# Optimization experiments

Hardware: AMD Instinct MI355X
Metric: run time of the kernel (lower is better)

## Reference

```python
import jax, jax.numpy as jnp
import numpy as np

B, T, D, HD = 256, 256, 512, 64  # batch, seq_len(SEQ_LEN), EMBED_DIM, head_dim


def setup_inputs() -> dict:
    key = jax.random.key(0)
    k1, k2, k3, k4 = jax.random.split(key, 4)
    scale = D ** -0.5  # roughly matches nn.Linear init variance
    return {
        "x": jax.random.normal(k1, (B, T, D), dtype=jnp.float32),
        "Wq": jax.random.normal(k2, (HD, D), dtype=jnp.float32) * scale,
        "Wk": jax.random.normal(k3, (HD, D), dtype=jnp.float32) * scale,
        "Wv": jax.random.normal(k4, (HD, D), dtype=jnp.float32) * scale,
    }


def reference(x, Wq, Wk, Wv):
    # q,k,v: [B, T, HD]  (torch Linear: x @ W.T, no bias)
    q = jnp.einsum("btd,hd->bth", x, Wq)
    k = jnp.einsum("btd,hd->bth", x, Wk)
    v = jnp.einsum("btd,hd->bth", x, Wv)
    head_dim = Wq.shape[0]
    # scores: [B, T, T], scaled by head_dim^-0.5
    scores = jnp.einsum("bqh,bkh->bqk", q, k) * (head_dim ** -0.5)
    T_ = x.shape[1]
    causal = jnp.tril(jnp.ones((T_, T_), dtype=bool))  # tril[:T,:T] == 0 -> -inf
    scores = jnp.where(causal, scores, -jnp.inf)
    attn = jax.nn.softmax(scores, axis=-1)
    # dropout is identity in eval mode (reference baseline)
    return jnp.einsum("bqk,bkh->bqh", attn, v)
```

## Files before the change

### kernel.cpp

```cpp
#include <hip/hip_runtime.h>
#include <hip/hip_bf16.h>
#include <stdint.h>

#define NB 256
#define NT 256
#define ND 512
#define NH 64

typedef __bf16 bf16;
typedef __bf16 bf16x4 __attribute__((ext_vector_type(4)));
typedef __bf16 bf16x8 __attribute__((ext_vector_type(8)));
typedef float f32x4 __attribute__((ext_vector_type(4)));

static __device__ __forceinline__ f32x4 mfma16(bf16x8 a, bf16x8 b, f32x4 c) {
    return __builtin_amdgcn_mfma_f32_16x16x32_bf16(a, b, c, 0, 0, 0);
}

static __device__ __forceinline__ bf16x8 cvt8(f32x4 a, f32x4 b) {
    bf16x8 r;
    r[0] = (bf16)a.x; r[1] = (bf16)a.y; r[2] = (bf16)a.z; r[3] = (bf16)a.w;
    r[4] = (bf16)b.x; r[5] = (bf16)b.y; r[6] = (bf16)b.z; r[7] = (bf16)b.w;
    return r;
}

static __device__ __forceinline__ void gload_lds16(const void* g, void* l) {
    __builtin_amdgcn_global_load_lds(
        (const __attribute__((address_space(1))) void*)g,
        (__attribute__((address_space(3))) void*)l, 16, 0, 0);
}

__global__ __launch_bounds__(256) void wconv_kernel(
        const float* __restrict__ Wq, const float* __restrict__ Wk,
        const float* __restrict__ Wv, bf16* __restrict__ wbf) {
    int idx = (blockIdx.x * 256 + threadIdx.x) * 4;
    const float* src;
    if (idx < 64 * ND)       src = Wq + idx;
    else if (idx < 128 * ND) src = Wk + (idx - 64 * ND);
    else                     src = Wv + (idx - 128 * ND);
    f32x4 v = *reinterpret_cast<const f32x4*>(src);
    bf16x4 o;
    o[0] = (bf16)v.x; o[1] = (bf16)v.y; o[2] = (bf16)v.z; o[3] = (bf16)v.w;
    *reinterpret_cast<bf16x4*>(wbf + idx) = o;
}

__global__ __launch_bounds__(256, 4) void qkv_gemm_kernel(
        const float* __restrict__ x, const bf16* __restrict__ wbf,
        bf16* __restrict__ qws, bf16* __restrict__ kws, bf16* __restrict__ vt) {
    __shared__ alignas(16) char lds[32768];
    const int t = threadIdx.x, lane = t & 63, wave = t >> 6;
    const int l15 = lane & 15, g = lane >> 4;
    const long m0 = (long)blockIdx.x * 64;
    const char* xb = (const char*)x;

    f32x4 acc[4][3] = {};

    #pragma unroll
    for (int i = 0; i < 4; ++i) {
        int row = wave * 16 + i * 4 + g;
        const char* src = xb + (m0 + row) * 2048 + ((l15 * 16) ^ ((row & 7) << 4));
        gload_lds16(src, lds + (wave * 4 + i) * 1024);
    }
    asm volatile("s_waitcnt vmcnt(0)");
    __syncthreads();

    #pragma unroll
    for (int s = 0; s < 8; ++s) {
        const int cbuf = (s & 1) * 16384;
        if (s < 7) {
            const int nbuf = ((s + 1) & 1) * 16384;
            #pragma unroll
            for (int i = 0; i < 4; ++i) {
                int row = wave * 16 + i * 4 + g;
                const char* src = xb + (m0 + row) * 2048 + (long)(s + 1) * 256
                                + ((l15 * 16) ^ ((row & 7) << 4));
                gload_lds16(src, lds + nbuf + (wave * 4 + i) * 1024);
            }
        }
        #pragma unroll
        for (int k2 = 0; k2 < 2; ++k2) {
            const int cbyte = (k2 * 32 + g * 8) * 4;
            bf16x8 Af[4];
            #pragma unroll
            for (int ri = 0; ri < 4; ++ri) {
                int row = ri * 16 + l15;
                int sw = (row & 7) << 4;
                f32x4 lo = *reinterpret_cast<const f32x4*>(lds + cbuf + row * 256 + (cbyte ^ sw));
                f32x4 hi = *reinterpret_cast<const f32x4*>(lds + cbuf + row * 256 + ((cbyte + 16) ^ sw));
                Af[ri] = cvt8(lo, hi);
            }
            const int kg = s * 64 + k2 * 32 + g * 8;
            #pragma unroll
            for (int ci = 0; ci < 3; ++ci) {
                int n = wave * 48 + ci * 16 + l15;
                bf16x8 Bf = *reinterpret_cast<const bf16x8*>(wbf + n * ND + kg);
                #pragma unroll
                for (int ri = 0; ri < 4; ++ri)
                    acc[ri][ci] = mfma16(Af[ri], Bf, acc[ri][ci]);
            }
        }
        asm volatile("s_waitcnt vmcnt(0)");
        __syncthreads();
    }

    const int b = blockIdx.x >> 2;
    const int tb = (blockIdx.x & 3) * 64;
    #pragma unroll
    for (int ci = 0; ci < 3; ++ci) {
        int n = wave * 48 + ci * 16 + l15;
        int sel = n >> 6, hd = n & 63;
        #pragma unroll
        for (int ri = 0; ri < 4; ++ri) {
            #pragma unroll
            for (int r = 0; r < 4; ++r) {
                int trow = tb + ri * 16 + g * 4 + r;
                long grow = m0 + ri * 16 + g * 4 + r;
                float val = acc[ri][ci][r];
                if (sel == 0)      qws[grow * NH + hd] = (bf16)(val * 0.125f);
                else if (sel == 1) kws[grow * NH + hd] = (bf16)val;
                else               vt[((long)b * NH + hd) * NT + trow] = (bf16)val;
            }
        }
    }
}

__global__ __launch_bounds__(256) void attn_kernel(
        const bf16* __restrict__ qws, const bf16* __restrict__ kws,
        const bf16* __restrict__ vt, float* __restrict__ out) {
    __shared__ alignas(16) char lds[65536];
    const int t = threadIdx.x, lane = t & 63, wave = t >> 6;
    const int l15 = lane & 15, g = lane >> 4;
    const int b = blockIdx.x;
    const long bbase = (long)b * NT;

    {
        const bf16* src = kws + (bbase + t) * NH;
        char* dstrow = lds + t * 128;
        int sw = (t & 7) << 4;
        #pragma unroll
        for (int j = 0; j < 8; ++j) {
            bf16x8 v = *reinterpret_cast<const bf16x8*>(src + j * 8);
            *reinterpret_cast<bf16x8*>(dstrow + ((j * 16) ^ sw)) = v;
        }
    }
    __syncthreads();

    char* plds = lds + 32768 + wave * 8192;
    const int qts[4] = {wave, 7 - wave, 8 + wave, 15 - wave};

    #pragma unroll
    for (int qi = 0; qi < 4; ++qi) {
        const int qt = qts[qi];
        const int nct = qt + 1, nch = (nct + 1) >> 1;
        bf16x8 Qf0, Qf1;
        {
            const bf16* qsrc = qws + (bbase + qt * 16 + l15) * NH + g * 8;
            Qf0 = *reinterpret_cast<const bf16x8*>(qsrc);
            Qf1 = *reinterpret_cast<const bf16x8*>(qsrc + 32);
        }
        const int qrow0 = qt * 16 + g * 4;
        float sum[4] = {0.f, 0.f, 0.f, 0.f};
        f32x4 O[4] = {};

        for (int ch = 0; ch < nch; ++ch) {
            const int c0 = ch * 32 + l15;
            const int c1 = c0 + 16;
            const bool t1v = (2 * ch + 1) < nct;
            f32x4 S0 = {}, S1 = {};
            {
                const char* k0p = lds + c0 * 128;
                int sw0 = (c0 & 7) << 4;
                S0 = mfma16(Qf0, *reinterpret_cast<const bf16x8*>(k0p + ((g * 16) ^ sw0)), S0);
                S0 = mfma16(Qf1, *reinterpret_cast<const bf16x8*>(k0p + ((64 + g * 16) ^ sw0)), S0);
                if (t1v) {
                    const char* k1p = lds + c1 * 128;
                    int sw1 = (c1 & 7) << 4;
                    S1 = mfma16(Qf0, *reinterpret_cast<const bf16x8*>(k1p + ((g * 16) ^ sw1)), S1);
                    S1 = mfma16(Qf1, *reinterpret_cast<const bf16x8*>(k1p + ((64 + g * 16) ^ sw1)), S1);
                }
            }
            #pragma unroll
            for (int r = 0; r < 4; ++r) {
                int rowp = g * 4 + r;
                int swp = (rowp & 7) << 4;
                float p0 = (c0 <= qrow0 + r) ? __expf(S0[r]) : 0.0f;
                sum[r] += p0;
                *reinterpret_cast<bf16*>(plds + ((rowp * 512 + c0 * 2) ^ swp)) = (bf16)p0;
                float p1 = (t1v && c1 <= qrow0 + r) ? __expf(S1[r]) : 0.0f;
                sum[r] += p1;
                *reinterpret_cast<bf16*>(plds + ((rowp * 512 + c1 * 2) ^ swp)) = (bf16)p1;
            }
            const int k0 = ch * 32 + g * 8;
            bf16x8 Pf = *reinterpret_cast<const bf16x8*>(
                plds + ((l15 * 512 + k0 * 2) ^ ((l15 & 7) << 4)));
            #pragma unroll
            for (int cb2 = 0; cb2 < 4; ++cb2) {
                int hd = cb2 * 16 + l15;
                bf16x8 Vf = *reinterpret_cast<const bf16x8*>(
                    vt + ((long)b * NH + hd) * NT + k0);
                O[cb2] = mfma16(Pf, Vf, O[cb2]);
            }
        }

        #pragma unroll
        for (int r = 0; r < 4; ++r) {
            sum[r] += __shfl_xor(sum[r], 1);
            sum[r] += __shfl_xor(sum[r], 2);
            sum[r] += __shfl_xor(sum[r], 4);
            sum[r] += __shfl_xor(sum[r], 8);
            sum[r] = 1.0f / sum[r];
        }
        #pragma unroll
        for (int cb2 = 0; cb2 < 4; ++cb2) {
            int hd = cb2 * 16 + l15;
            #pragma unroll
            for (int r = 0; r < 4; ++r) {
                long orow = bbase + qt * 16 + g * 4 + r;
                out[orow * NH + hd] = O[cb2][r] * sum[r];
            }
        }
    }
}

extern "C" void kernel_launch(void* const* d_in, const int* in_sizes, int n_in,
                              void* d_out, int out_size, void* d_ws, size_t ws_size,
                              hipStream_t stream) {
    const float* x  = (const float*)d_in[0];
    const float* Wq = (const float*)d_in[1];
    const float* Wk = (const float*)d_in[2];
    const float* Wv = (const float*)d_in[3];
    float* out = (float*)d_out;

    char* ws = (char*)d_ws;
    bf16* wbf = (bf16*)ws;
    bf16* qws = (bf16*)(ws + 0x30000);
    bf16* kws = (bf16*)(ws + 0x30000 + 8388608);
    bf16* vt  = (bf16*)(ws + 0x30000 + 2 * 8388608);

    wconv_kernel<<<96, 256, 0, stream>>>(Wq, Wk, Wv, wbf);
    qkv_gemm_kernel<<<1024, 256, 0, stream>>>(x, wbf, qws, kws, vt);
    attn_kernel<<<NB, 256, 0, stream>>>(qws, kws, vt, out);
}
```

Baseline: 231.6 us.

## Triple-buffer QKV GEMM with prefetched weights and split attention across query blocks

The QKV projection GEMM moves from double to triple LDS buffering with two stages in flight and a partial vmcnt wait. Weight fragments for the next stage are prefetched into registers instead of being loaded inside the MFMA loop. The attention kernel now launches a 4xB grid so each block handles one 64-row query block and loads only the causal prefix of K. Its P scratch shrinks to a 1KB per-wave tile, which lowers LDS use and allows more blocks per CU. Splitting attention this way gives up K reuse across query blocks and leaves some load imbalance between blocks, in exchange for four times as many blocks to fill the GPU.

```diff
diff --git a/kernel.cpp b/kernel.cpp
--- a/kernel.cpp
+++ b/kernel.cpp
@@ -43,39 +43,49 @@
     *reinterpret_cast<bf16x4*>(wbf + idx) = o;
 }
 
-__global__ __launch_bounds__(256, 4) void qkv_gemm_kernel(
+__global__ __launch_bounds__(256, 3) void qkv_gemm_kernel(
         const float* __restrict__ x, const bf16* __restrict__ wbf,
         bf16* __restrict__ qws, bf16* __restrict__ kws, bf16* __restrict__ vt) {
-    __shared__ alignas(16) char lds[32768];
+    __shared__ alignas(16) char lds[49152];
     const int t = threadIdx.x, lane = t & 63, wave = t >> 6;
     const int l15 = lane & 15, g = lane >> 4;
     const long m0 = (long)blockIdx.x * 64;
     const char* xb = (const char*)x;
 
     f32x4 acc[4][3] = {};
-
-    #pragma unroll
-    for (int i = 0; i < 4; ++i) {
-        int row = wave * 16 + i * 4 + g;
-        const char* src = xb + (m0 + row) * 2048 + ((l15 * 16) ^ ((row & 7) << 4));
-        gload_lds16(src, lds + (wave * 4 + i) * 1024);
-    }
-    asm volatile("s_waitcnt vmcnt(0)");
-    __syncthreads();
+    bf16x8 Wcur[6], Wnxt[6];
+
+    auto stageDMA = [&](int s) {
+        char* base = lds + (s % 3) * 16384;
+        #pragma unroll
+        for (int i = 0; i < 4; ++i) {
+            int row = wave * 16 + i * 4 + g;
+            const char* src = xb + (m0 + row) * 2048 + (long)s * 256
+                            + ((l15 * 16) ^ ((row & 7) << 4));
+            gload_lds16(src, base + (wave * 4 + i) * 1024);
+        }
+    };
+    auto loadW = [&](int s, bf16x8* Wr) {
+        #pragma unroll
+        for (int ci = 0; ci < 3; ++ci) {
+            int n = wave * 48 + ci * 16 + l15;
+            const bf16* wsrc = wbf + n * ND + s * 64 + g * 8;
+            Wr[ci * 2 + 0] = *reinterpret_cast<const bf16x8*>(wsrc);
+            Wr[ci * 2 + 1] = *reinterpret_cast<const bf16x8*>(wsrc + 32);
+        }
+    };
+
+    loadW(0, Wcur);
+    stageDMA(0);
+    stageDMA(1);
+    asm volatile("s_waitcnt vmcnt(4)" ::: "memory");
+    __builtin_amdgcn_s_barrier();
 
     #pragma unroll
     for (int s = 0; s < 8; ++s) {
-        const int cbuf = (s & 1) * 16384;
-        if (s < 7) {
-            const int nbuf = ((s + 1) & 1) * 16384;
-            #pragma unroll
-            for (int i = 0; i < 4; ++i) {
-                int row = wave * 16 + i * 4 + g;
-                const char* src = xb + (m0 + row) * 2048 + (long)(s + 1) * 256
-                                + ((l15 * 16) ^ ((row & 7) << 4));
-                gload_lds16(src, lds + nbuf + (wave * 4 + i) * 1024);
-            }
-        }
+        if (s < 7) loadW(s + 1, Wnxt);
+        if (s < 6) stageDMA(s + 2);
+        char* cbuf = lds + (s % 3) * 16384;
         #pragma unroll
         for (int k2 = 0; k2 < 2; ++k2) {
             const int cbyte = (k2 * 32 + g * 8) * 4;
@@ -84,22 +94,24 @@
             for (int ri = 0; ri < 4; ++ri) {
                 int row = ri * 16 + l15;
                 int sw = (row & 7) << 4;
-                f32x4 lo = *reinterpret_cast<const f32x4*>(lds + cbuf + row * 256 + (cbyte ^ sw));
-                f32x4 hi = *reinterpret_cast<const f32x4*>(lds + cbuf + row * 256 + ((cbyte + 16) ^ sw));
+                f32x4 lo = *reinterpret_cast<const f32x4*>(cbuf + row * 256 + (cbyte ^ sw));
+                f32x4 hi = *reinterpret_cast<const f32x4*>(cbuf + row * 256 + ((cbyte + 16) ^ sw));
                 Af[ri] = cvt8(lo, hi);
             }
-            const int kg = s * 64 + k2 * 32 + g * 8;
             #pragma unroll
             for (int ci = 0; ci < 3; ++ci) {
-                int n = wave * 48 + ci * 16 + l15;
-                bf16x8 Bf = *reinterpret_cast<const bf16x8*>(wbf + n * ND + kg);
                 #pragma unroll
                 for (int ri = 0; ri < 4; ++ri)
-                    acc[ri][ci] = mfma16(Af[ri], Bf, acc[ri][ci]);
-            }
-        }
-        asm volatile("s_waitcnt vmcnt(0)");
-        __syncthreads();
+                    acc[ri][ci] = mfma16(Af[ri], Wcur[ci * 2 + k2], acc[ri][ci]);
+            }
+        }
+        if (s < 7) {
+            #pragma unroll
+            for (int i = 0; i < 6; ++i) Wcur[i] = Wnxt[i];
+            asm volatile("s_waitcnt vmcnt(4)" ::: "memory");
+            __builtin_amdgcn_s_barrier();
+            asm volatile("" ::: "memory");
+        }
     }
 
     const int b = blockIdx.x >> 2;
@@ -123,16 +135,17 @@
     }
 }
 
-__global__ __launch_bounds__(256) void attn_kernel(
+__global__ __launch_bounds__(256, 4) void attn_kernel(
         const bf16* __restrict__ qws, const bf16* __restrict__ kws,
         const bf16* __restrict__ vt, float* __restrict__ out) {
-    __shared__ alignas(16) char lds[65536];
+    __shared__ alignas(16) char lds[36864];
     const int t = threadIdx.x, lane = t & 63, wave = t >> 6;
     const int l15 = lane & 15, g = lane >> 4;
-    const int b = blockIdx.x;
+    const int qb = blockIdx.x, b = blockIdx.y;
     const long bbase = (long)b * NT;
-
-    {
+    const int KV = (qb + 1) * 64;
+
+    if (t < KV) {
         const bf16* src = kws + (bbase + t) * NH;
         char* dstrow = lds + t * 128;
         int sw = (t & 7) << 4;
@@ -144,79 +157,74 @@
     }
     __syncthreads();
 
-    char* plds = lds + 32768 + wave * 8192;
-    const int qts[4] = {wave, 7 - wave, 8 + wave, 15 - wave};
-
-    #pragma unroll
-    for (int qi = 0; qi < 4; ++qi) {
-        const int qt = qts[qi];
-        const int nct = qt + 1, nch = (nct + 1) >> 1;
-        bf16x8 Qf0, Qf1;
+    const int qt = qb * 4 + wave;
+    const int nct = qt + 1, nch = (nct + 1) >> 1;
+    char* plds = lds + 32768 + wave * 1024;
+
+    bf16x8 Qf0, Qf1;
+    {
+        const bf16* qsrc = qws + (bbase + qt * 16 + l15) * NH + g * 8;
+        Qf0 = *reinterpret_cast<const bf16x8*>(qsrc);
+        Qf1 = *reinterpret_cast<const bf16x8*>(qsrc + 32);
+    }
+    const int qrow0 = qt * 16 + g * 4;
+    float sum[4] = {0.f, 0.f, 0.f, 0.f};
+    f32x4 O[4] = {};
+
+    for (int ch = 0; ch < nch; ++ch) {
+        const int c0 = ch * 32 + l15, c1 = c0 + 16;
+        const bool t1v = (2 * ch + 1) < nct;
+        f32x4 S0 = {}, S1 = {};
         {
-            const bf16* qsrc = qws + (bbase + qt * 16 + l15) * NH + g * 8;
-            Qf0 = *reinterpret_cast<const bf16x8*>(qsrc);
-            Qf1 = *reinterpret_cast<const bf16x8*>(qsrc + 32);
-        }
-        const int qrow0 = qt * 16 + g * 4;
-        float sum[4] = {0.f, 0.f, 0.f, 0.f};
-        f32x4 O[4] = {};
-
-        for (int ch = 0; ch < nch; ++ch) {
-            const int c0 = ch * 32 + l15;
-            const int c1 = c0 + 16;
-            const bool t1v = (2 * ch + 1) < nct;
-            f32x4 S0 = {}, S1 = {};
-            {
-                const char* k0p = lds + c0 * 128;
-                int sw0 = (c0 & 7) << 4;
-                S0 = mfma16(Qf0, *reinterpret_cast<const bf16x8*>(k0p + ((g * 16) ^ sw0)), S0);
-                S0 = mfma16(Qf1, *reinterpret_cast<const bf16x8*>(k0p + ((64 + g * 16) ^ sw0)), S0);
-                if (t1v) {
-                    const char* k1p = lds + c1 * 128;
-                    int sw1 = (c1 & 7) << 4;
-                    S1 = mfma16(Qf0, *reinterpret_cast<const bf16x8*>(k1p + ((g * 16) ^ sw1)), S1);
-                    S1 = mfma16(Qf1, *reinterpret_cast<const bf16x8*>(k1p + ((64 + g * 16) ^ sw1)), S1);
-                }
-            }
-            #pragma unroll
-            for (int r = 0; r < 4; ++r) {
-                int rowp = g * 4 + r;
-                int swp = (rowp & 7) << 4;
-                float p0 = (c0 <= qrow0 + r) ? __expf(S0[r]) : 0.0f;
-                sum[r] += p0;
-                *reinterpret_cast<bf16*>(plds + ((rowp * 512 + c0 * 2) ^ swp)) = (bf16)p0;
-                float p1 = (t1v && c1 <= qrow0 + r) ? __expf(S1[r]) : 0.0f;
-                sum[r] += p1;
-                *reinterpret_cast<bf16*>(plds + ((rowp * 512 + c1 * 2) ^ swp)) = (bf16)p1;
-            }
-            const int k0 = ch * 32 + g * 8;
-            bf16x8 Pf = *reinterpret_cast<const bf16x8*>(
-                plds + ((l15 * 512 + k0 * 2) ^ ((l15 & 7) << 4)));
-            #pragma unroll
-            for (int cb2 = 0; cb2 < 4; ++cb2) {
-                int hd = cb2 * 16 + l15;
-                bf16x8 Vf = *reinterpret_cast<const bf16x8*>(
-                    vt + ((long)b * NH + hd) * NT + k0);
-                O[cb2] = mfma16(Pf, Vf, O[cb2]);
-            }
-        }
-
+            const char* k0p = lds + c0 * 128;
+            int sw0 = (c0 & 7) << 4;
+            S0 = mfma16(Qf0, *reinterpret_cast<const bf16x8*>(k0p + ((g * 16) ^ sw0)), S0);
+            S0 = mfma16(Qf1, *reinterpret_cast<const bf16x8*>(k0p + ((64 + g * 16) ^ sw0)), S0);
+            if (t1v) {
+                const char* k1p = lds + c1 * 128;
+                int sw1 = (c1 & 7) << 4;
+                S1 = mfma16(Qf0, *reinterpret_cast<const bf16x8*>(k1p + ((g * 16) ^ sw1)), S1);
+                S1 = mfma16(Qf1, *reinterpret_cast<const bf16x8*>(k1p + ((64 + g * 16) ^ sw1)), S1);
+            }
+        }
         #pragma unroll
         for (int r = 0; r < 4; ++r) {
-            sum[r] += __shfl_xor(sum[r], 1);
-            sum[r] += __shfl_xor(sum[r], 2);
-            sum[r] += __shfl_xor(sum[r], 4);
-            sum[r] += __shfl_xor(sum[r], 8);
-            sum[r] = 1.0f / sum[r];
-        }
+            int rowp = g * 4 + r;
+            int key = ((rowp >> 2) & 3) << 4;
+            float p0 = (c0 <= qrow0 + r) ? __expf(S0[r]) : 0.0f;
+            sum[r] += p0;
+            *reinterpret_cast<bf16*>(plds + rowp * 64 + ((2 * l15) ^ key)) = (bf16)p0;
+            float p1 = (t1v && c1 <= qrow0 + r) ? __expf(S1[r]) : 0.0f;
+            sum[r] += p1;
+            *reinterpret_cast<bf16*>(plds + rowp * 64 + ((2 * (l15 + 16)) ^ key)) = (bf16)p1;
+        }
+        bf16x8 Pf = *reinterpret_cast<const bf16x8*>(
+            plds + l15 * 64 + ((g * 16) ^ (((l15 >> 2) & 3) << 4)));
+        const int k0 = ch * 32 + g * 8;
         #pragma unroll
         for (int cb2 = 0; cb2 < 4; ++cb2) {
             int hd = cb2 * 16 + l15;
-            #pragma unroll
-            for (int r = 0; r < 4; ++r) {
-                long orow = bbase + qt * 16 + g * 4 + r;
-                out[orow * NH + hd] = O[cb2][r] * sum[r];
-            }
+            bf16x8 Vf = *reinterpret_cast<const bf16x8*>(
+                vt + ((long)b * NH + hd) * NT + k0);
+            O[cb2] = mfma16(Pf, Vf, O[cb2]);
+        }
+    }
+
+    #pragma unroll
+    for (int r = 0; r < 4; ++r) {
+        sum[r] += __shfl_xor(sum[r], 1);
+        sum[r] += __shfl_xor(sum[r], 2);
+        sum[r] += __shfl_xor(sum[r], 4);
+        sum[r] += __shfl_xor(sum[r], 8);
+        sum[r] = 1.0f / sum[r];
+    }
+    #pragma unroll
+    for (int cb2 = 0; cb2 < 4; ++cb2) {
+        int hd = cb2 * 16 + l15;
+        #pragma unroll
+        for (int r = 0; r < 4; ++r) {
+            long orow = bbase + qt * 16 + g * 4 + r;
+            out[orow * NH + hd] = O[cb2][r] * sum[r];
         }
     }
 }
@@ -238,5 +246,5 @@
 
     wconv_kernel<<<96, 256, 0, stream>>>(Wq, Wk, Wv, wbf);
     qkv_gemm_kernel<<<1024, 256, 0, stream>>>(x, wbf, qws, kws, vt);
-    attn_kernel<<<NB, 256, 0, stream>>>(qws, kws, vt, out);
-}
+    attn_kernel<<<dim3(4, NB), 256, 0, stream>>>(qws, kws, vt, out);
+}
```

After: 239.6 us. 1.03x slower.
